# Performance work log

Hardware: AMD Instinct MI355X
Metric: run time of the kernel (lower is better)

Reference implementation:

```python
import jax, jax.numpy as jnp
import numpy as np

N_HEAD = 16

def setup_inputs() -> dict:
    key = jax.random.key(0)
    k1, k2, k3 = jax.random.split(key, 3)
    B, T, C = 4, 2048, 1024
    x = jax.random.normal(k1, (B, T, C), dtype=jnp.float32)
    w_qkv = jax.random.normal(k2, (C, 3 * C), dtype=jnp.float32) * (C ** -0.5)
    w_out = jax.random.normal(k3, (C, C), dtype=jnp.float32) * (C ** -0.5)
    return {"x": x, "w_qkv": w_qkv, "w_out": w_out}

def reference(x, w_qkv, w_out):
    B, T, C = x.shape
    H = N_HEAD
    d_k = C // H
    scale = d_k ** -0.5
    qkv = (x @ w_qkv).reshape(B, T, 3, H, d_k)
    q = qkv[:, :, 0].transpose(0, 2, 1, 3)  # [B,H,T,d_k]
    k = qkv[:, :, 1].transpose(0, 2, 1, 3)
    v = qkv[:, :, 2].transpose(0, 2, 1, 3)
    scores = jnp.einsum('bhqd,bhkd->bhqk', q, k) * scale  # [B,H,T,T]
    causal = jnp.tril(jnp.ones((T, T), dtype=bool))
    scores = jnp.where(causal[None, None], scores, jnp.finfo(scores.dtype).min)
    probs = jax.nn.softmax(scores, axis=-1)
    out = jnp.einsum('bhqk,bhkd->bhqd', probs, v)  # [B,H,T,d_k]
    out = out.transpose(0, 2, 1, 3).reshape(B, T, C)
    return out @ w_out
```

## Files before the change

kernel.cpp:

```cpp
#include <hip/hip_runtime.h>
#include <stdint.h>


typedef __bf16 bf16_t;
typedef __bf16 bf16x4 __attribute__((ext_vector_type(4)));
typedef __bf16 bf16x8 __attribute__((ext_vector_type(8)));
typedef float f32x4 __attribute__((ext_vector_type(4)));

#define LOG2E 1.44269504088896340736f
#define QSCALE (0.125f * LOG2E)

__device__ __forceinline__ void gl_lds16(const void* g, void* l) {
  __builtin_amdgcn_global_load_lds(
      (const __attribute__((address_space(1))) unsigned int*)g,
      (__attribute__((address_space(3))) unsigned int*)l, 16, 0, 0);
}

__device__ __forceinline__ f32x4 mfma16(bf16x8 a, bf16x8 b, f32x4 c) {
  return __builtin_amdgcn_mfma_f32_16x16x32_bf16(a, b, c, 0, 0, 0);
}

__global__ __launch_bounds__(256) void k_cvt_bf16(const float* __restrict__ in,
                                                  bf16_t* __restrict__ out, int n4) {
  int i = blockIdx.x * 256 + threadIdx.x;
  int step = gridDim.x * 256;
  for (; i < n4; i += step) {
    f32x4 v = reinterpret_cast<const f32x4*>(in)[i];
    bf16x4 o;
    o[0] = (bf16_t)v[0]; o[1] = (bf16_t)v[1];
    o[2] = (bf16_t)v[2]; o[3] = (bf16_t)v[3];
    reinterpret_cast<bf16x4*>(out)[i] = o;
  }
}

__global__ __launch_bounds__(256) void k_transpose_cvt2(const float* __restrict__ w_qkv,
                                                        const float* __restrict__ w_out,
                                                        bf16_t* __restrict__ outq,
                                                        bf16_t* __restrict__ outo) {
  __shared__ float tile[64][65];
  const int tid = threadIdx.x;
  const int bx = blockIdx.x;
  const float* in = (bx < 48) ? w_qkv : w_out;
  bf16_t* out = (bx < 48) ? outq : outo;
  const int Cc = (bx < 48) ? 3072 : 1024;
  const int c0 = ((bx < 48) ? bx : bx - 48) * 64;
  const int R = 1024;
  const int r0 = blockIdx.y * 64;
  const int rr = tid >> 4, cc = (tid & 15) * 4;
#pragma unroll
  for (int i = 0; i < 4; i++) {
    f32x4 v = *reinterpret_cast<const f32x4*>(&in[(size_t)(r0 + rr + i * 16) * Cc + c0 + cc]);
    tile[rr + i * 16][cc + 0] = v[0];
    tile[rr + i * 16][cc + 1] = v[1];
    tile[rr + i * 16][cc + 2] = v[2];
    tile[rr + i * 16][cc + 3] = v[3];
  }
  __syncthreads();
  const int cr = tid >> 2, kb = (tid & 3) * 16;
#pragma unroll
  for (int j4 = 0; j4 < 4; j4++) {
    bf16x4 o;
#pragma unroll
    for (int jj = 0; jj < 4; jj++) o[jj] = (bf16_t)tile[kb + j4 * 4 + jj][cr];
    *reinterpret_cast<bf16x4*>(&out[(size_t)(c0 + cr) * R + r0 + kb + j4 * 4]) = o;
  }
}

__global__ __launch_bounds__(256) void k_transpose_v(const bf16_t* __restrict__ v,
                                                     bf16_t* __restrict__ vT) {
  __shared__ bf16_t tile[64 * 64];
  const int tid = threadIdx.x;
  const int bh = blockIdx.y;
  const int b = bh >> 4, h = bh & 15;
  const int t0 = blockIdx.x * 64;
#pragma unroll
  for (int i = 0; i < 2; i++) {
    int c = tid + 256 * i;
    int tl = c >> 3, ch = c & 7;
    bf16x8 val = *reinterpret_cast<const bf16x8*>(
        &v[(size_t)(b * 2048 + t0 + tl) * 1024 + h * 64 + ch * 8]);
    int sw = (ch ^ (tl & 7) ^ (tl >> 3)) & 7;
    *reinterpret_cast<bf16x8*>(&tile[tl * 64 + sw * 8]) = val;
  }
  __syncthreads();
#pragma unroll
  for (int i = 0; i < 2; i++) {
    int c = tid + 256 * i;
    int d = c >> 3, tc = c & 7;
    bf16x8 o;
#pragma unroll
    for (int j = 0; j < 8; j++) {
      int t = tc * 8 + j;
      int sw = ((d >> 3) ^ (t & 7) ^ (t >> 3)) & 7;
      o[j] = tile[t * 64 + sw * 8 + (d & 7)];
    }
    *reinterpret_cast<bf16x8*>(&vT[((size_t)bh * 64 + d) * 2048 + t0 + tc * 8]) = o;
  }
}

template <int MODE>
__global__ __launch_bounds__(256) void k_gemm(const bf16_t* __restrict__ A,
                                              const bf16_t* __restrict__ Bt,
                                              void* __restrict__ C0, void* __restrict__ C1,
                                              int M, int N, int K, int nbx) {
  constexpr int BM = 128, BN = 128, BK = 32;
  __shared__ bf16_t a_sh[3][BM * BK];
  __shared__ bf16_t b_sh[3][BN * BK];
  const int tid = threadIdx.x;
  const int wave = tid >> 6, lane = tid & 63;
  const int g = lane >> 4, lr = lane & 15;
  const int wm = wave >> 1, wn = wave & 1;
  const int nblk = gridDim.x;
  const int swid = (blockIdx.x & 7) * (nblk >> 3) + (blockIdx.x >> 3);
  const int m0 = (swid / nbx) * BM, n0 = (swid % nbx) * BN;

  const bf16_t* ag[2];
  const bf16_t* bg[2];
#pragma unroll
  for (int i = 0; i < 2; i++) {
    int c = tid + 256 * i;
    int row = c >> 2, ch = c & 3;
    int chs = ch ^ ((row >> 1) & 3);
    ag[i] = A + (size_t)(m0 + row) * K + chs * 8;
    bg[i] = Bt + (size_t)(n0 + row) * K + chs * 8;
  }

  f32x4 acc[4][4];
#pragma unroll
  for (int i = 0; i < 4; i++)
#pragma unroll
    for (int j = 0; j < 4; j++) acc[i][j] = (f32x4){0.f, 0.f, 0.f, 0.f};

  auto stage = [&](int buf) {
#pragma unroll
    for (int i = 0; i < 2; i++) {
      gl_lds16(ag[i], &a_sh[buf][(tid + 256 * i) * 8]);
      gl_lds16(bg[i], &b_sh[buf][(tid + 256 * i) * 8]);
      ag[i] += BK;
      bg[i] += BK;
    }
  };

  stage(0);
  stage(1);
  const int nK = K / BK;
  const int swz = (lr >> 1) & 3;
  int buf = 0;
  for (int it = 0; it < nK; ++it) {
    if (it < nK - 1) asm volatile("s_waitcnt vmcnt(4)" ::: "memory");
    else             asm volatile("s_waitcnt vmcnt(0)" ::: "memory");
    __builtin_amdgcn_s_barrier();
    asm volatile("" ::: "memory");
    if (it + 2 < nK) stage(buf >= 1 ? buf - 1 : buf + 2);

    bf16x8 af[4], bfr[4];
#pragma unroll
    for (int mi = 0; mi < 4; mi++)
      af[mi] = *reinterpret_cast<const bf16x8*>(
          &a_sh[buf][(wm * 64 + mi * 16 + lr) * BK + (g ^ swz) * 8]);
#pragma unroll
    for (int ni = 0; ni < 4; ni++)
      bfr[ni] = *reinterpret_cast<const bf16x8*>(
          &b_sh[buf][(wn * 64 + ni * 16 + lr) * BK + (g ^ swz) * 8]);
    __builtin_amdgcn_s_setprio(1);
#pragma unroll
    for (int mi = 0; mi < 4; mi++)
#pragma unroll
      for (int ni = 0; ni < 4; ni++) acc[mi][ni] = mfma16(af[mi], bfr[ni], acc[mi][ni]);
    __builtin_amdgcn_s_setprio(0);
    asm volatile("" ::: "memory");
    buf = (buf < 2) ? buf + 1 : 0;
  }

#pragma unroll
  for (int mi = 0; mi < 4; mi++) {
#pragma unroll
    for (int ni = 0; ni < 4; ni++) {
      const int mb = m0 + wm * 64 + mi * 16 + g * 4;
      const int nb = n0 + wn * 64 + ni * 16;
      if constexpr (MODE == 2) {
        float* C = (float*)C0;
#pragma unroll
        for (int r = 0; r < 4; r++) C[(size_t)(mb + r) * N + nb + lr] = acc[mi][ni][r];
      } else {
        if (nb < 2048) {
          const float scl = (nb < 1024) ? QSCALE : 1.0f;
          bf16_t* qk = (bf16_t*)C0;
#pragma unroll
          for (int r = 0; r < 4; r++)
            qk[(size_t)(mb + r) * 2048 + nb + lr] = (bf16_t)(acc[mi][ni][r] * scl);
        } else {
          bf16_t* vb = (bf16_t*)C1;
#pragma unroll
          for (int r = 0; r < 4; r++)
            vb[(size_t)(mb + r) * 1024 + (nb - 2048) + lr] = (bf16_t)acc[mi][ni][r];
        }
      }
    }
  }
}

__global__ __launch_bounds__(256) void k_attn(const bf16_t* __restrict__ qk,
                                              const bf16_t* __restrict__ vT,
                                              bf16_t* __restrict__ out) {
  constexpr int T = 2048;
  constexpr int PST = 72;
  __shared__ bf16_t k_sh[3][64 * 64];
  __shared__ bf16_t v_sh[3][64 * 64];
  __shared__ bf16_t p_sh[4][32 * PST];
  const int tid = threadIdx.x;
  const int wave = tid >> 6, lane = tid & 63;
  const int g = lane >> 4, lr = lane & 15;

  const int flat = blockIdx.x;
  const int qt = 15 - (flat >> 6);
  const int s6 = flat & 63;
  const int bh = (s6 & 7) * 8 + (s6 >> 3);
  const int b = bh >> 4, h = bh & 15;
  const int q0w = qt * 128 + wave * 32;

  bf16x8 qf[2][2];
#pragma unroll
  for (int rb = 0; rb < 2; rb++) {
    const bf16_t* Qr = qk + (size_t)(b * T + q0w + rb * 16 + lr) * 2048 + h * 64;
    qf[rb][0] = *reinterpret_cast<const bf16x8*>(Qr + g * 8);
    qf[rb][1] = *reinterpret_cast<const bf16x8*>(Qr + 32 + g * 8);
  }

  f32x4 acc_o[2][4];
#pragma unroll
  for (int rb = 0; rb < 2; rb++)
#pragma unroll
    for (int dt = 0; dt < 4; dt++) acc_o[rb][dt] = (f32x4){0.f, 0.f, 0.f, 0.f};
  float mrow[2] = {-1e30f, -1e30f};
  float lrow[2] = {0.f, 0.f};

  const int nt = 2 * qt + 2;

  const bf16_t* kg[2];
  const bf16_t* vg[2];
  {
    const bf16_t* Kbase = qk + (size_t)b * T * 2048 + 1024 + h * 64;
    const bf16_t* Vbase = vT + (size_t)bh * 64 * T;
#pragma unroll
    for (int i = 0; i < 2; i++) {
      int c = tid + 256 * i;
      int row = c >> 3, col8 = (c & 7) ^ (row & 7);
      kg[i] = Kbase + (size_t)row * 2048 + col8 * 8;
      vg[i] = Vbase + (size_t)row * T + col8 * 8;
    }
  }

  auto stageT = [&](int bufn) {
#pragma unroll
    for (int i = 0; i < 2; i++) {
      gl_lds16(kg[i], &k_sh[bufn][(tid + 256 * i) * 8]);
      gl_lds16(vg[i], &v_sh[bufn][(tid + 256 * i) * 8]);
      kg[i] += 64 * 2048;
      vg[i] += 64;
    }
  };

  stageT(0);
  stageT(1);

  int buf = 0;
  for (int t = 0; t < nt; ++t) {
    const int kv0 = t * 64;
    if (t < nt - 1) asm volatile("s_waitcnt vmcnt(4)" ::: "memory");
    else            asm volatile("s_waitcnt vmcnt(0)" ::: "memory");
    __builtin_amdgcn_s_barrier();
    asm volatile("" ::: "memory");
    if (t + 2 < nt) stageT(buf >= 1 ? buf - 1 : buf + 2);

    if (kv0 <= q0w + 31) {
      f32x4 s[2][4];
#pragma unroll
      for (int rb = 0; rb < 2; rb++)
#pragma unroll
        for (int kt = 0; kt < 4; kt++) s[rb][kt] = (f32x4){0.f, 0.f, 0.f, 0.f};
      __builtin_amdgcn_s_setprio(1);
#pragma unroll
      for (int kt = 0; kt < 4; kt++) {
        const int row = kt * 16 + lr, sw = row & 7;
        bf16x8 kf0 = *reinterpret_cast<const bf16x8*>(&k_sh[buf][row * 64 + (g ^ sw) * 8]);
        bf16x8 kf1 = *reinterpret_cast<const bf16x8*>(&k_sh[buf][row * 64 + ((4 + g) ^ sw) * 8]);
#pragma unroll
        for (int rb = 0; rb < 2; rb++) {
          s[rb][kt] = mfma16(kf0, qf[rb][0], s[rb][kt]);
          s[rb][kt] = mfma16(kf1, qf[rb][1], s[rb][kt]);
        }
      }
      __builtin_amdgcn_s_setprio(0);

      if (kv0 + 63 > q0w) {
#pragma unroll
        for (int rb = 0; rb < 2; rb++)
#pragma unroll
          for (int kt = 0; kt < 4; kt++)
#pragma unroll
            for (int r = 0; r < 4; r++)
              if (kv0 + kt * 16 + g * 4 + r > q0w + rb * 16 + lr) s[rb][kt][r] = -1e30f;
      }

#pragma unroll
      for (int rb = 0; rb < 2; rb++) {
        float pm = s[rb][0][0];
#pragma unroll
        for (int kt = 0; kt < 4; kt++)
#pragma unroll
          for (int r = 0; r < 4; r++) pm = fmaxf(pm, s[rb][kt][r]);
        pm = fmaxf(pm, __shfl_xor(pm, 16, 64));
        pm = fmaxf(pm, __shfl_xor(pm, 32, 64));

        unsigned long long need = __ballot(pm > mrow[rb] + 8.0f);
        if (need) {
          float mnew = fmaxf(mrow[rb], pm);
          float alpha = __builtin_amdgcn_exp2f(mrow[rb] - mnew);
          mrow[rb] = mnew;
          lrow[rb] *= alpha;
#pragma unroll
          for (int r = 0; r < 4; r++) {
            int src = (lane & 48) | ((lane >> 2) & 12) | r;
            float ar = __shfl(alpha, src, 64);
#pragma unroll
            for (int dt = 0; dt < 4; dt++) acc_o[rb][dt][r] *= ar;
          }
        }

        float rs = 0.f;
#pragma unroll
        for (int kt = 0; kt < 4; kt++) {
          f32x4 p;
#pragma unroll
          for (int r = 0; r < 4; r++) p[r] = __builtin_amdgcn_exp2f(s[rb][kt][r] - mrow[rb]);
          rs += (p[0] + p[1]) + (p[2] + p[3]);
          bf16x4 pb;
#pragma unroll
          for (int r = 0; r < 4; r++) pb[r] = (bf16_t)p[r];
          *reinterpret_cast<bf16x4*>(&p_sh[wave][(rb * 16 + lr) * PST + kt * 16 + g * 4]) = pb;
        }
        rs += __shfl_xor(rs, 16, 64);
        rs += __shfl_xor(rs, 32, 64);
        lrow[rb] += rs;
      }

      bf16x8 pa[2][2];
#pragma unroll
      for (int rb = 0; rb < 2; rb++) {
        pa[rb][0] = *reinterpret_cast<const bf16x8*>(&p_sh[wave][(rb * 16 + lr) * PST + g * 8]);
        pa[rb][1] =
            *reinterpret_cast<const bf16x8*>(&p_sh[wave][(rb * 16 + lr) * PST + 32 + g * 8]);
      }
      __builtin_amdgcn_s_setprio(1);
#pragma unroll
      for (int dt = 0; dt < 4; dt++) {
        const int drow = dt * 16 + lr, sw = drow & 7;
        bf16x8 v0 = *reinterpret_cast<const bf16x8*>(&v_sh[buf][drow * 64 + (g ^ sw) * 8]);
        bf16x8 v1 = *reinterpret_cast<const bf16x8*>(&v_sh[buf][drow * 64 + ((4 + g) ^ sw) * 8]);
#pragma unroll
        for (int rb = 0; rb < 2; rb++) {
          acc_o[rb][dt] = mfma16(pa[rb][0], v0, acc_o[rb][dt]);
          acc_o[rb][dt] = mfma16(pa[rb][1], v1, acc_o[rb][dt]);
        }
      }
      __builtin_amdgcn_s_setprio(0);
    }
    asm volatile("" ::: "memory");
    buf = (buf < 2) ? buf + 1 : 0;
  }

#pragma unroll
  for (int rb = 0; rb < 2; rb++) {
    const float linv = 1.0f / lrow[rb];
#pragma unroll
    for (int r = 0; r < 4; r++) {
      int src = (lane & 48) | ((lane >> 2) & 12) | r;
      float lq = __shfl(linv, src, 64);
#pragma unroll
      for (int dt = 0; dt < 4; dt++)
        out[(size_t)(b * T + q0w + rb * 16 + g * 4 + r) * 1024 + h * 64 + dt * 16 + lr] =
            (bf16_t)(acc_o[rb][dt][r] * lq);
    }
  }
}

extern "C" void kernel_launch(void* const* d_in, const int* in_sizes, int n_in,
                              void* d_out, int out_size, void* d_ws, size_t ws_size,
                              hipStream_t stream) {
  (void)in_sizes; (void)n_in; (void)out_size; (void)ws_size;
  const float* x = (const float*)d_in[0];
  const float* w_qkv = (const float*)d_in[1];
  const float* w_out = (const float*)d_in[2];
  float* out = (float*)d_out;
  const int T = 2048, C = 1024;
  const int M = 4 * T;

  bf16_t* xb = (bf16_t*)d_ws;
  bf16_t* wqkvT = xb + (size_t)M * C;
  bf16_t* woutT = wqkvT + (size_t)3 * C * C;
  bf16_t* qkbuf = woutT + (size_t)C * C;
  bf16_t* vbuf = qkbuf + (size_t)M * 2 * C;
  bf16_t* vT = vbuf + (size_t)M * C;

  k_cvt_bf16<<<2048, 256, 0, stream>>>(x, xb, M * C / 4);
  k_transpose_cvt2<<<dim3(64, 16), 256, 0, stream>>>(w_qkv, w_out, wqkvT, woutT);
  k_gemm<1><<<(3 * C / 128) * (M / 128), 256, 0, stream>>>(xb, wqkvT, qkbuf, vbuf, M, 3 * C, C,
                                                           3 * C / 128);
  k_transpose_v<<<dim3(32, 64), 256, 0, stream>>>(vbuf, vT);
  k_attn<<<1024, 256, 0, stream>>>(qkbuf, vT, vbuf);
  k_gemm<2><<<(C / 128) * (M / 128), 256, 0, stream>>>(vbuf, woutT, out, nullptr, M, C, C,
                                                       C / 128);
}
```

Measured before the change: 259.6 us.

## Add dedicated 256x256-tile QKV GEMM kernel with 8 waves and double-buffered LDS

Replaces the generic 128x128 GEMM for the QKV projection with a specialized kernel using 256x256 output tiles, 512 threads (8 waves, each computing 128x64), and a K-step of 64 split into two 32-wide halves. It double-buffers A/B tiles in LDS with interleaved global-to-LDS loads between MFMA groups and explicit vmcnt waits. The aim is higher arithmetic intensity and better overlap of loads with MFMAs. The cost is much larger LDS use (128KB) and high register pressure, which may limit occupancy. The old QKV epilogue in k_gemm is removed.

```diff
diff --git a/kernel.cpp b/kernel.cpp
--- a/kernel.cpp
+++ b/kernel.cpp
@@ -95,6 +95,134 @@
       o[j] = tile[t * 64 + sw * 8 + (d & 7)];
     }
     *reinterpret_cast<bf16x8*>(&vT[((size_t)bh * 64 + d) * 2048 + t0 + tc * 8]) = o;
+  }
+}
+
+__global__ __launch_bounds__(512, 2) void k_gemmqkv(const bf16_t* __restrict__ A,
+                                                    const bf16_t* __restrict__ Bt,
+                                                    bf16_t* __restrict__ qk,
+                                                    bf16_t* __restrict__ vb, int nbx) {
+  constexpr int K = 1024;
+  __shared__ bf16_t a0[2 * 8192];
+  __shared__ bf16_t b0[2 * 8192];
+  __shared__ bf16_t a1[2 * 8192];
+  __shared__ bf16_t b1[2 * 8192];
+  const int tid = threadIdx.x;
+  const int wave = tid >> 6, lane = tid & 63;
+  const int g = lane >> 4, lr = lane & 15;
+  const int wm = wave >> 2, wn = wave & 3;
+  const int nblk = gridDim.x;
+  const int swid = (blockIdx.x & 7) * (nblk >> 3) + (blockIdx.x >> 3);
+  const int m0 = (swid / nbx) * 256, n0 = (swid % nbx) * 256;
+
+  const bf16_t* pA0 = A + (size_t)(m0 + (tid >> 2)) * K + (tid & 3) * 8;
+  const bf16_t* pA1 = A + (size_t)(m0 + ((tid + 512) >> 2)) * K + ((tid + 512) & 3) * 8;
+  const bf16_t* pB0 = Bt + (size_t)(n0 + (tid >> 2)) * K + (tid & 3) * 8;
+  const bf16_t* pB1 = Bt + (size_t)(n0 + ((tid + 512) >> 2)) * K + ((tid + 512) & 3) * 8;
+
+  f32x4 acc[8][4];
+#pragma unroll
+  for (int i = 0; i < 8; i++)
+#pragma unroll
+    for (int j = 0; j < 4; j++) acc[i][j] = (f32x4){0.f, 0.f, 0.f, 0.f};
+
+  auto stageA = [&](bf16_t* sa, int kh, int kt) {
+    gl_lds16(pA0 + kt * 64 + kh * 32, sa + kh * 8192 + tid * 8);
+    gl_lds16(pA1 + kt * 64 + kh * 32, sa + kh * 8192 + (tid + 512) * 8);
+  };
+  auto stageB = [&](bf16_t* sb, int kh, int kt) {
+    gl_lds16(pB0 + kt * 64 + kh * 32, sb + kh * 8192 + tid * 8);
+    gl_lds16(pB1 + kt * 64 + kh * 32, sb + kh * 8192 + (tid + 512) * 8);
+  };
+
+  const int arow = wm * 128 + lr;
+  const int bcol = wn * 64 + lr;
+
+  auto tile_step = [&](const bf16_t* ra, const bf16_t* rb, bf16_t* sa, bf16_t* sb,
+                       int kts, bool doS) {
+    asm volatile("s_waitcnt vmcnt(4)" ::: "memory");
+    __builtin_amdgcn_s_barrier();
+    bf16x8 bfr[4], af[4];
+    if (doS) stageA(sa, 0, kts);
+#pragma unroll
+    for (int nt = 0; nt < 4; nt++)
+      bfr[nt] = *reinterpret_cast<const bf16x8*>(rb + (bcol + nt * 16) * 32 + g * 8);
+#pragma unroll
+    for (int mt = 0; mt < 4; mt++)
+      af[mt] = *reinterpret_cast<const bf16x8*>(ra + (arow + mt * 16) * 32 + g * 8);
+    __builtin_amdgcn_s_setprio(1);
+#pragma unroll
+    for (int mt = 0; mt < 4; mt++)
+#pragma unroll
+      for (int nt = 0; nt < 4; nt++) acc[mt][nt] = mfma16(af[mt], bfr[nt], acc[mt][nt]);
+    __builtin_amdgcn_s_setprio(0);
+    if (doS) stageB(sb, 0, kts);
+#pragma unroll
+    for (int mt = 0; mt < 4; mt++)
+      af[mt] = *reinterpret_cast<const bf16x8*>(ra + (arow + (mt + 4) * 16) * 32 + g * 8);
+    __builtin_amdgcn_s_setprio(1);
+#pragma unroll
+    for (int mt = 0; mt < 4; mt++)
+#pragma unroll
+      for (int nt = 0; nt < 4; nt++)
+        acc[mt + 4][nt] = mfma16(af[mt], bfr[nt], acc[mt + 4][nt]);
+    __builtin_amdgcn_s_setprio(0);
+    if (doS) asm volatile("s_waitcnt vmcnt(4)" ::: "memory");
+    else     asm volatile("s_waitcnt vmcnt(0)" ::: "memory");
+    __builtin_amdgcn_s_barrier();
+    if (doS) stageA(sa, 1, kts);
+#pragma unroll
+    for (int nt = 0; nt < 4; nt++)
+      bfr[nt] = *reinterpret_cast<const bf16x8*>(rb + 8192 + (bcol + nt * 16) * 32 + g * 8);
+#pragma unroll
+    for (int mt = 0; mt < 4; mt++)
+      af[mt] = *reinterpret_cast<const bf16x8*>(ra + 8192 + (arow + mt * 16) * 32 + g * 8);
+    __builtin_amdgcn_s_setprio(1);
+#pragma unroll
+    for (int mt = 0; mt < 4; mt++)
+#pragma unroll
+      for (int nt = 0; nt < 4; nt++) acc[mt][nt] = mfma16(af[mt], bfr[nt], acc[mt][nt]);
+    __builtin_amdgcn_s_setprio(0);
+    if (doS) stageB(sb, 1, kts);
+#pragma unroll
+    for (int mt = 0; mt < 4; mt++)
+      af[mt] = *reinterpret_cast<const bf16x8*>(ra + 8192 + (arow + (mt + 4) * 16) * 32 + g * 8);
+    __builtin_amdgcn_s_setprio(1);
+#pragma unroll
+    for (int mt = 0; mt < 4; mt++)
+#pragma unroll
+      for (int nt = 0; nt < 4; nt++)
+        acc[mt + 4][nt] = mfma16(af[mt], bfr[nt], acc[mt + 4][nt]);
+    __builtin_amdgcn_s_setprio(0);
+  };
+
+  stageA(a0, 0, 0);
+  stageB(b0, 0, 0);
+  stageA(a0, 1, 0);
+  stageB(b0, 1, 0);
+
+  for (int it = 0; it < 8; ++it) {
+    tile_step(a0, b0, a1, b1, 2 * it + 1, true);
+    tile_step(a1, b1, a0, b0, 2 * it + 2, it < 7);
+  }
+
+#pragma unroll
+  for (int mt = 0; mt < 8; mt++) {
+#pragma unroll
+    for (int nt = 0; nt < 4; nt++) {
+      const int mb = m0 + wm * 128 + mt * 16 + g * 4;
+      const int nb = n0 + wn * 64 + nt * 16;
+      if (nb < 2048) {
+        const float scl = (nb < 1024) ? QSCALE : 1.0f;
+#pragma unroll
+        for (int r = 0; r < 4; r++)
+          qk[(size_t)(mb + r) * 2048 + nb + lr] = (bf16_t)(acc[mt][nt][r] * scl);
+      } else {
+#pragma unroll
+        for (int r = 0; r < 4; r++)
+          vb[(size_t)(mb + r) * 1024 + (nb - 2048) + lr] = (bf16_t)acc[mt][nt][r];
+      }
+    }
   }
 }
 
@@ -183,18 +311,7 @@
 #pragma unroll
         for (int r = 0; r < 4; r++) C[(size_t)(mb + r) * N + nb + lr] = acc[mi][ni][r];
       } else {
-        if (nb < 2048) {
-          const float scl = (nb < 1024) ? QSCALE : 1.0f;
-          bf16_t* qk = (bf16_t*)C0;
-#pragma unroll
-          for (int r = 0; r < 4; r++)
-            qk[(size_t)(mb + r) * 2048 + nb + lr] = (bf16_t)(acc[mi][ni][r] * scl);
-        } else {
-          bf16_t* vb = (bf16_t*)C1;
-#pragma unroll
-          for (int r = 0; r < 4; r++)
-            vb[(size_t)(mb + r) * 1024 + (nb - 2048) + lr] = (bf16_t)acc[mi][ni][r];
-        }
+        (void)C1;
       }
     }
   }
@@ -405,8 +522,7 @@
 
   k_cvt_bf16<<<2048, 256, 0, stream>>>(x, xb, M * C / 4);
   k_transpose_cvt2<<<dim3(64, 16), 256, 0, stream>>>(w_qkv, w_out, wqkvT, woutT);
-  k_gemm<1><<<(3 * C / 128) * (M / 128), 256, 0, stream>>>(xb, wqkvT, qkbuf, vbuf, M, 3 * C, C,
-                                                           3 * C / 128);
+  k_gemmqkv<<<(M / 256) * (3 * C / 256), 512, 0, stream>>>(xb, wqkvT, qkbuf, vbuf, 3 * C / 256);
   k_transpose_v<<<dim3(32, 64), 256, 0, stream>>>(vbuf, vT);
   k_attn<<<1024, 256, 0, stream>>>(qkbuf, vT, vbuf);
   k_gemm<2><<<(C / 128) * (M / 128), 256, 0, stream>>>(vbuf, woutT, out, nullptr, M, C, C,
```

Measured after the change: 263.9 us. Within noise of the previous version (+1.7%).
